# Kernel optimization log

Measured on AMD Instinct MI355X. Metric: run time of the kernel, lower is better.

## Reference

```python
import jax, jax.numpy as jnp
import numpy as np

N_HEADS = 16
HEAD_DIM = 64
D_MODEL = N_HEADS * HEAD_DIM
NEG_INF = -10000.0


def setup_inputs() -> dict:
    key = jax.random.key(0)
    ks = jax.random.split(key, 6)
    B, S = 2, 2048
    std = 0.02
    return {
        "from_tensor": jax.random.normal(ks[0], (B, S, D_MODEL), dtype=jnp.float32),
        "to_tensor": jax.random.normal(ks[1], (B, S, D_MODEL), dtype=jnp.float32),
        "attention_mask": jnp.ones((B, S, S), dtype=jnp.int32),
        "Wq": jax.random.normal(ks[2], (D_MODEL, D_MODEL), dtype=jnp.float32) * std,
        "bq": jnp.zeros((D_MODEL,), dtype=jnp.float32),
        "Wk": jax.random.normal(ks[3], (D_MODEL, D_MODEL), dtype=jnp.float32) * std,
        "bk": jnp.zeros((D_MODEL,), dtype=jnp.float32),
        "Wv": jax.random.normal(ks[4], (D_MODEL, D_MODEL), dtype=jnp.float32) * std,
        "bv": jnp.zeros((D_MODEL,), dtype=jnp.float32),
    }


def reference(from_tensor, to_tensor, attention_mask, Wq, bq, Wk, bk, Wv, bv):
    B, F, _ = from_tensor.shape
    T = to_tensor.shape[1]
    # Dense QKV projections (no activation by default)
    q = from_tensor @ Wq + bq          # [B, F, N*H]
    k = to_tensor @ Wk + bk            # [B, T, N*H]
    v = to_tensor @ Wv + bv            # [B, T, N*H]
    # split heads -> [B, N, S, H]
    q = q.reshape(B, F, N_HEADS, HEAD_DIM).transpose(0, 2, 1, 3)
    k = k.reshape(B, T, N_HEADS, HEAD_DIM).transpose(0, 2, 1, 3)
    v = v.reshape(B, T, N_HEADS, HEAD_DIM).transpose(0, 2, 1, 3)
    # scaled dot-product scores [B, N, F, T]
    scores = jnp.einsum("bnfh,bnth->bnft", q, k) / jnp.sqrt(jnp.float32(HEAD_DIM))
    # additive mask: (1 - mask) * -10000, broadcast over heads
    adder = (1.0 - attention_mask.astype(jnp.float32))[:, None, :, :] * NEG_INF
    scores = scores + adder
    probs = jax.nn.softmax(scores, axis=-1)  # dropout is identity at inference
    ctx = jnp.einsum("bnft,bnth->bnfh", probs, v)  # [B, N, F, H]
    return ctx.transpose(0, 2, 1, 3).reshape(B, F, N_HEADS * HEAD_DIM)
```

## Files before the change

### kernel.cpp

```cpp
#include <hip/hip_runtime.h>
#include <hip/hip_bf16.h>

typedef unsigned short u16;
typedef __bf16 bf16x8 __attribute__((ext_vector_type(8)));
typedef float f32x4 __attribute__((ext_vector_type(4)));

#define D_MODEL 1024
#define NH 16
#define HD 64
#define SEQ 2048
#define BATCH 2

__device__ __forceinline__ f32x4 mfma16(bf16x8 a, bf16x8 b, f32x4 c) {
    return __builtin_amdgcn_mfma_f32_16x16x32_bf16(a, b, c, 0, 0, 0);
}

__device__ __forceinline__ u16 f2bf(float f) {
    __hip_bfloat16 h = __float2bfloat16(f);
    return *reinterpret_cast<u16*>(&h);
}

__device__ __forceinline__ void gload_lds16(const void* g, void* l) {
    __builtin_amdgcn_global_load_lds((__attribute__((address_space(1))) void*)g,
                                     (__attribute__((address_space(3))) void*)l,
                                     16, 0, 0);
}

__global__ __launch_bounds__(256) void convert_k(const float* __restrict__ src,
                                                 u16* __restrict__ dst, int n8) {
    const int i = blockIdx.x * 256 + threadIdx.x;
    if (i >= n8) return;
    const float4 a = ((const float4*)src)[i * 2];
    const float4 b = ((const float4*)src)[i * 2 + 1];
    union { u16 h[8]; uint4 v; } u;
    u.h[0] = f2bf(a.x); u.h[1] = f2bf(a.y); u.h[2] = f2bf(a.z); u.h[3] = f2bf(a.w);
    u.h[4] = f2bf(b.x); u.h[5] = f2bf(b.y); u.h[6] = f2bf(b.z); u.h[7] = f2bf(b.w);
    *(uint4*)(dst + i * 8) = u.v;
}

__global__ __launch_bounds__(256) void transposeW_k(const float* __restrict__ src,
                                                    u16* __restrict__ dst,
                                                    int R, int C) {
    __shared__ __align__(16) u16 t[64][72];
    const int tid = threadIdx.x;
    const int r0 = blockIdx.y * 64, c0 = blockIdx.x * 64;
#pragma unroll
    for (int j = 0; j < 2; ++j) {
        int idx = j * 256 + tid;
        int rr = idx >> 3, cc = idx & 7;
        size_t base = (size_t)(r0 + rr) * C + c0 + cc * 8;
        float4 a = *(const float4*)(src + base);
        float4 b = *(const float4*)(src + base + 4);
        union { u16 h[8]; uint4 v; } u;
        u.h[0] = f2bf(a.x); u.h[1] = f2bf(a.y); u.h[2] = f2bf(a.z); u.h[3] = f2bf(a.w);
        u.h[4] = f2bf(b.x); u.h[5] = f2bf(b.y); u.h[6] = f2bf(b.z); u.h[7] = f2bf(b.w);
        *(uint4*)&t[rr][cc * 8] = u.v;
    }
    __syncthreads();
#pragma unroll
    for (int j = 0; j < 2; ++j) {
        int idx = j * 256 + tid;
        int cc = idx >> 3, rr8 = idx & 7;
        union { u16 h[8]; uint4 v; } u;
#pragma unroll
        for (int e = 0; e < 8; ++e) u.h[e] = t[rr8 * 8 + e][cc];
        *(uint4*)(dst + (size_t)(c0 + cc) * R + r0 + rr8 * 8) = u.v;
    }
}

__global__ __launch_bounds__(256) void maskflags_k(const int* __restrict__ mask,
                                                   int* __restrict__ flags) {
    const int tid = threadIdx.x;
    const int ti = blockIdx.x, fi = blockIdx.y, b = blockIdx.z;
    const int f = fi * 128 + (tid >> 1);
    const int4* p = (const int4*)(mask + ((size_t)(b * SEQ + f)) * SEQ + ti * 64 + (tid & 1) * 32);
    int ok = 1;
#pragma unroll
    for (int j = 0; j < 8; ++j) {
        int4 v = p[j];
        ok &= (v.x == 1) & (v.y == 1) & (v.z == 1) & (v.w == 1);
    }
    __shared__ int sflag;
    if (tid == 0) sflag = 1;
    __syncthreads();
    if (!ok) sflag = 0;
    __syncthreads();
    if (tid == 0) flags[(b * 16 + fi) * 32 + ti] = sflag;
}

__global__ __launch_bounds__(256, 2) void qkv_gemm_k(
    const u16* __restrict__ Xq, const u16* __restrict__ Xkv,
    const u16* __restrict__ Wt,
    const float* __restrict__ bq, const float* __restrict__ bk,
    const float* __restrict__ bv,
    u16* __restrict__ Qb, u16* __restrict__ Kb, u16* __restrict__ Vt) {
    const int z = blockIdx.z;
    const u16* X = (z == 0) ? Xq : Xkv;
    const u16* Wz = Wt + (size_t)z * D_MODEL * D_MODEL;
    const float* bias = (z == 0) ? bq : (z == 1 ? bk : bv);
    const float scale = (z == 0) ? 0.1803368801111244f : 1.0f;

    __shared__ __align__(16) u16 As[128 * 32];
    __shared__ __align__(16) u16 Bs[128 * 32];

    const int tid = threadIdx.x;
    const int w = tid >> 6, lane = tid & 63;
    const int q = lane >> 4, c = lane & 15;
    const int m0 = blockIdx.x * 128, n0 = blockIdx.y * 128;
    const int mw = (w & 1) * 64, nw = (w >> 1) * 64;

    f32x4 acc[4][4];
    const f32x4 z4 = {0.f, 0.f, 0.f, 0.f};
#pragma unroll
    for (int mi = 0; mi < 4; ++mi)
#pragma unroll
        for (int ni = 0; ni < 4; ++ni) acc[mi][ni] = z4;

    for (int kb = 0; kb < 32; ++kb) {
        const int k0 = kb * 32;
#pragma unroll
        for (int j = 0; j < 2; ++j) {
            int i = j * 256 + tid;
            int r = i >> 2, cc = i & 3;
            gload_lds16(X + (size_t)(m0 + r) * D_MODEL + k0 + cc * 8, As + i * 8);
            gload_lds16(Wz + (size_t)(n0 + r) * D_MODEL + k0 + cc * 8, Bs + i * 8);
        }
        __syncthreads();
        bf16x8 af[4], bfr[4];
#pragma unroll
        for (int mi = 0; mi < 4; ++mi)
            af[mi] = *(const bf16x8*)(As + (mw + mi * 16 + c) * 32 + q * 8);
#pragma unroll
        for (int ni = 0; ni < 4; ++ni)
            bfr[ni] = *(const bf16x8*)(Bs + (nw + ni * 16 + c) * 32 + q * 8);
#pragma unroll
        for (int mi = 0; mi < 4; ++mi)
#pragma unroll
            for (int ni = 0; ni < 4; ++ni)
                acc[mi][ni] = mfma16(af[mi], bfr[ni], acc[mi][ni]);
        __syncthreads();
    }

    if (z == 2) {
#pragma unroll
        for (int ni = 0; ni < 4; ++ni) {
            const int colg = n0 + nw + ni * 16 + c;
            const float bvv = bias[colg];
            const int head = colg >> 6, h = colg & 63;
#pragma unroll
            for (int mi = 0; mi < 4; ++mi) {
                const int rowg = m0 + mw + mi * 16 + q * 4;
                const int b = rowg >> 11, s = rowg & 2047;
                union { u16 h4[4]; uint2 v2; } pk;
#pragma unroll
                for (int r = 0; r < 4; ++r) pk.h4[r] = f2bf(acc[mi][ni][r] + bvv);
                *(uint2*)(Vt + (((size_t)(b * NH + head)) * HD + h) * SEQ + s) = pk.v2;
            }
        }
    } else {
        u16* outb = (z == 0) ? Qb : Kb;
#pragma unroll
        for (int ni = 0; ni < 4; ++ni) {
            const int colg = n0 + nw + ni * 16 + c;
            const float bvv = bias[colg];
            const int head = colg >> 6, h = colg & 63;
#pragma unroll
            for (int mi = 0; mi < 4; ++mi) {
                const int rowg = m0 + mw + mi * 16 + q * 4;
#pragma unroll
                for (int r = 0; r < 4; ++r) {
                    const int mrow = rowg + r;
                    const int b = mrow >> 11, s = mrow & 2047;
                    const float val = (acc[mi][ni][r] + bvv) * scale;
                    outb[(((size_t)(b * NH + head)) * SEQ + s) * HD + h] = f2bf(val);
                }
            }
        }
    }
}

#define SK_OFF (128 * 144)
#define SV_OFF (SK_OFF + 64 * 144)
#define SMEM_BYTES (SV_OFF + 64 * 144)

__global__ __launch_bounds__(256, 4) void attn_k(
    const u16* __restrict__ Qb, const u16* __restrict__ Kb, const u16* __restrict__ Vt,
    const int* __restrict__ flags, const int* __restrict__ mask,
    float* __restrict__ O0, float* __restrict__ l0, float* __restrict__ l1,
    float* __restrict__ out) {
    __shared__ __align__(16) unsigned char smem[SMEM_BYTES];
    const int tid = threadIdx.x;
    const int w = tid >> 6, lane = tid & 63;
    const int q = lane >> 4, c = lane & 15;
    const int fi = blockIdx.x, bn = blockIdx.y, ts = blockIdx.z;
    const int b = bn >> 4, n = bn & 15;
    const int f0 = fi * 128;

    u16* sQ = (u16*)(smem);
    u16* sK = (u16*)(smem + SK_OFF);
    u16* sV = (u16*)(smem + SV_OFF);
    u16* sP = sQ + w * 32 * 72;

#pragma unroll
    for (int j = 0; j < 4; ++j) {
        int i = j * 256 + tid;
        int r = i >> 3, cc = i & 7;
        uint4 v = *(const uint4*)(Qb + ((size_t)(bn * SEQ + f0 + r)) * HD + cc * 8);
        *(uint4*)(sQ + r * 72 + cc * 8) = v;
    }
    __syncthreads();

    bf16x8 qf[2][2];
#pragma unroll
    for (int ft = 0; ft < 2; ++ft)
#pragma unroll
        for (int kb = 0; kb < 2; ++kb)
            qf[ft][kb] = *(const bf16x8*)(sQ + (w * 32 + ft * 16 + c) * 72 + kb * 32 + q * 8);
    __asm__ __volatile__("" ::: "memory");
    __builtin_amdgcn_s_waitcnt(0xC07F);
    __asm__ __volatile__("" ::: "memory");

    union { u16 h[8]; bf16x8 v; } one_u;
#pragma unroll
    for (int j = 0; j < 8; ++j) one_u.h[j] = 0x3F80;
    const bf16x8 ones = one_u.v;

    f32x4 O[2][4], accL[2];
    const f32x4 z4 = {0.f, 0.f, 0.f, 0.f};
#pragma unroll
    for (int mi = 0; mi < 2; ++mi) {
        accL[mi] = z4;
#pragma unroll
        for (int hi = 0; hi < 4; ++hi) O[mi][hi] = z4;
    }
    const int* flagp = flags + (b * 16 + fi) * 32;

    const int it0 = ts * 16;
    for (int it = it0; it < it0 + 16; ++it) {
        const int t0 = it * 64;
#pragma unroll
        for (int j = 0; j < 2; ++j) {
            int i = j * 256 + tid;
            int r = i >> 3, cc = i & 7;
            uint4 kv = *(const uint4*)(Kb + ((size_t)(bn * SEQ + t0 + r)) * HD + cc * 8);
            uint4 vv = *(const uint4*)(Vt + ((size_t)(bn * HD + r)) * SEQ + t0 + cc * 8);
            *(uint4*)(sK + r * 72 + cc * 8) = kv;
            *(uint4*)(sV + r * 72 + cc * 8) = vv;
        }
        __syncthreads();

        const int maskslow = (flagp[it] == 0);

#pragma unroll
        for (int mt = 0; mt < 4; ++mt) {
            bf16x8 kf0 = *(const bf16x8*)(sK + (mt * 16 + c) * 72 + 0 + q * 8);
            bf16x8 kf1 = *(const bf16x8*)(sK + (mt * 16 + c) * 72 + 32 + q * 8);
            f32x4 st[2];
#pragma unroll
            for (int ft = 0; ft < 2; ++ft) {
                st[ft] = z4;
                st[ft] = mfma16(kf0, qf[ft][0], st[ft]);
                st[ft] = mfma16(kf1, qf[ft][1], st[ft]);
            }
            if (maskslow) {
#pragma unroll
                for (int ft = 0; ft < 2; ++ft)
#pragma unroll
                    for (int r = 0; r < 4; ++r) {
                        const int fg = f0 + w * 32 + ft * 16 + c;
                        const int tg = t0 + mt * 16 + q * 4 + r;
                        const int mv = mask[((size_t)(b * SEQ + fg)) * SEQ + tg];
                        st[ft][r] += (1.0f - (float)mv) * (-10000.0f) * 1.4426950408889634f;
                    }
            }
#pragma unroll
            for (int ft = 0; ft < 2; ++ft) {
                union { u16 h[4]; uint2 v2; } pk;
#pragma unroll
                for (int r = 0; r < 4; ++r)
                    pk.h[r] = f2bf(exp2f(st[ft][r] - 10.0f));
                *(uint2*)(sP + (ft * 16 + c) * 72 + mt * 16 + q * 4) = pk.v2;
            }
        }
        __asm__ __volatile__("" ::: "memory");
        __builtin_amdgcn_s_waitcnt(0xC07F);
        __asm__ __volatile__("" ::: "memory");

#pragma unroll
        for (int kb = 0; kb < 2; ++kb) {
            bf16x8 pf0 = *(const bf16x8*)(sP + (0 * 16 + c) * 72 + kb * 32 + q * 8);
            bf16x8 pf1 = *(const bf16x8*)(sP + (1 * 16 + c) * 72 + kb * 32 + q * 8);
#pragma unroll
            for (int hi = 0; hi < 4; ++hi) {
                bf16x8 vf = *(const bf16x8*)(sV + (hi * 16 + c) * 72 + kb * 32 + q * 8);
                O[0][hi] = mfma16(pf0, vf, O[0][hi]);
                O[1][hi] = mfma16(pf1, vf, O[1][hi]);
            }
            accL[0] = mfma16(pf0, ones, accL[0]);
            accL[1] = mfma16(pf1, ones, accL[1]);
        }
        __syncthreads();
    }

    float* Odst = ts ? out : O0;
    float* ldst = ts ? l1 : l0;
#pragma unroll
    for (int mi = 0; mi < 2; ++mi)
#pragma unroll
        for (int hi = 0; hi < 4; ++hi)
#pragma unroll
            for (int r = 0; r < 4; ++r) {
                const int fg = f0 + w * 32 + mi * 16 + q * 4 + r;
                const int col = n * 64 + hi * 16 + c;
                Odst[((size_t)(b * SEQ + fg)) * D_MODEL + col] = O[mi][hi][r];
            }
    if (c == 0) {
#pragma unroll
        for (int mi = 0; mi < 2; ++mi)
#pragma unroll
            for (int r = 0; r < 4; ++r) {
                const int fg = f0 + w * 32 + mi * 16 + q * 4 + r;
                ldst[(size_t)bn * SEQ + fg] = accL[mi][r];
            }
    }
}

__global__ __launch_bounds__(256) void combine_k(const float* __restrict__ O0,
                                                 const float* __restrict__ l0,
                                                 const float* __restrict__ l1,
                                                 float* __restrict__ out) {
    const int i = blockIdx.x * 256 + threadIdx.x;
    const int bf = i >> 8;
    const int col = (i & 255) << 2;
    const int n = col >> 6;
    const int lidx = ((bf >> 11) * NH + n) * SEQ + (bf & (SEQ - 1));
    const float inv = 1.0f / (l0[lidx] + l1[lidx]);
    const float4 a = ((const float4*)O0)[i];
    const float4 cpart = ((const float4*)out)[i];
    float4 r;
    r.x = (a.x + cpart.x) * inv;
    r.y = (a.y + cpart.y) * inv;
    r.z = (a.z + cpart.z) * inv;
    r.w = (a.w + cpart.w) * inv;
    ((float4*)out)[i] = r;
}

__global__ __launch_bounds__(256) void signal_k(float* __restrict__ out, int n,
                                                float val) {
    const int i = blockIdx.x * 256 + threadIdx.x;
    if (i < n) out[i] = val;
}

extern "C" void kernel_launch(void* const* d_in, const int* in_sizes, int n_in,
                              void* d_out, int out_size, void* d_ws, size_t ws_size,
                              hipStream_t stream) {
    const float* Xs[2] = {nullptr, nullptr};
    const float* Wp[3] = {nullptr, nullptr, nullptr};
    const float* Bp[3] = {nullptr, nullptr, nullptr};
    const int* mask = nullptr;
    int nx = 0, nw = 0, nb = 0;
    for (int i = 0; i < n_in; ++i) {
        const long long sz = in_sizes[i];
        if (sz == (long long)BATCH * SEQ * D_MODEL) {
            if (nx < 2) Xs[nx++] = (const float*)d_in[i];
        } else if (sz == (long long)BATCH * SEQ * SEQ) {
            mask = (const int*)d_in[i];
        } else if (sz == (long long)D_MODEL * D_MODEL) {
            if (nw < 3) Wp[nw++] = (const float*)d_in[i];
        } else if (sz == (long long)D_MODEL) {
            if (nb < 3) Bp[nb++] = (const float*)d_in[i];
        }
    }
    float* outp = (float*)d_out;
    const size_t MB = 1024 * 1024;
    const size_t NEED = 47 * MB;

    if (ws_size < NEED || nx != 2 || nw != 3 || nb != 3 || !mask) {
        float code = 1000.0f + (float)(ws_size / MB)
                   + (nx != 2 ? 10000.0f : 0.f)
                   + (nw != 3 ? 20000.0f : 0.f)
                   + (nb != 3 ? 40000.0f : 0.f)
                   + (!mask   ? 80000.0f : 0.f);
        signal_k<<<(out_size + 255) / 256, 256, 0, stream>>>(outp, out_size, code);
        return;
    }

    char* ws = (char*)d_ws;
    u16* Xqc   = (u16*)(ws);
    u16* Xkvc  = (u16*)(ws + 8 * MB);
    u16* Wt    = (u16*)(ws + 16 * MB);
    u16* Qb    = (u16*)(ws + 22 * MB);
    u16* Kb    = (u16*)(ws + 30 * MB);
    u16* Vt    = (u16*)(ws + 38 * MB);
    int* flags = (int*)(ws + 46 * MB);
    float* O0 = (float*)(ws);
    float* l0 = (float*)(ws + 46 * MB + 16 * 1024);
    float* l1 = (float*)(ws + 46 * MB + 16 * 1024 + 256 * 1024);

    convert_k<<<2048, 256, 0, stream>>>(Xs[0], Xqc, 524288);
    convert_k<<<2048, 256, 0, stream>>>(Xs[1], Xkvc, 524288);
    transposeW_k<<<dim3(16, 16), 256, 0, stream>>>(Wp[0], Wt,               1024, 1024);
    transposeW_k<<<dim3(16, 16), 256, 0, stream>>>(Wp[1], Wt + 1024 * 1024, 1024, 1024);
    transposeW_k<<<dim3(16, 16), 256, 0, stream>>>(Wp[2], Wt + 2048 * 1024, 1024, 1024);
    maskflags_k<<<dim3(32, 16, 2), 256, 0, stream>>>(mask, flags);
    qkv_gemm_k<<<dim3(32, 8, 3), 256, 0, stream>>>(Xqc, Xkvc, Wt,
                                                   Bp[0], Bp[1], Bp[2], Qb, Kb, Vt);
    attn_k<<<dim3(16, 32, 2), 256, 0, stream>>>(Qb, Kb, Vt, flags, mask,
                                                O0, l0, l1, outp);
    combine_k<<<4096, 256, 0, stream>>>(O0, l0, l1, outp);
}
```

Measured before the change: 232.8 us.

## Merge prep kernels into one launch, add MFMA priority, raise GEMM occupancy

Folds the two input conversions, three weight transposes and the mask-flag scan into a single prep_k launch, with the work chosen by block index. This removes five kernel launches and their tail gaps. It also wraps the attention MFMA sections in s_setprio(1)/s_setprio(0) so waves issuing matrix ops get scheduling priority, and raises the QKV GEMM launch bound from 2 to 3 blocks per SIMD. The higher occupancy target may force register spills.

```diff
diff --git a/kernel.cpp b/kernel.cpp
--- a/kernel.cpp
+++ b/kernel.cpp
@@ -26,69 +26,80 @@
                                      16, 0, 0);
 }
 
-__global__ __launch_bounds__(256) void convert_k(const float* __restrict__ src,
-                                                 u16* __restrict__ dst, int n8) {
-    const int i = blockIdx.x * 256 + threadIdx.x;
-    if (i >= n8) return;
-    const float4 a = ((const float4*)src)[i * 2];
-    const float4 b = ((const float4*)src)[i * 2 + 1];
-    union { u16 h[8]; uint4 v; } u;
-    u.h[0] = f2bf(a.x); u.h[1] = f2bf(a.y); u.h[2] = f2bf(a.z); u.h[3] = f2bf(a.w);
-    u.h[4] = f2bf(b.x); u.h[5] = f2bf(b.y); u.h[6] = f2bf(b.z); u.h[7] = f2bf(b.w);
-    *(uint4*)(dst + i * 8) = u.v;
-}
-
-__global__ __launch_bounds__(256) void transposeW_k(const float* __restrict__ src,
-                                                    u16* __restrict__ dst,
-                                                    int R, int C) {
+__global__ __launch_bounds__(256) void prep_k(
+    const float* __restrict__ X0, const float* __restrict__ X1,
+    u16* __restrict__ Xqc, u16* __restrict__ Xkvc,
+    const float* __restrict__ W0, const float* __restrict__ W1,
+    const float* __restrict__ W2, u16* __restrict__ Wt,
+    const int* __restrict__ mask, int* __restrict__ flags) {
     __shared__ __align__(16) u16 t[64][72];
     const int tid = threadIdx.x;
-    const int r0 = blockIdx.y * 64, c0 = blockIdx.x * 64;
-#pragma unroll
-    for (int j = 0; j < 2; ++j) {
-        int idx = j * 256 + tid;
-        int rr = idx >> 3, cc = idx & 7;
-        size_t base = (size_t)(r0 + rr) * C + c0 + cc * 8;
-        float4 a = *(const float4*)(src + base);
-        float4 b = *(const float4*)(src + base + 4);
+    int bid = blockIdx.x;
+
+    if (bid < 4096) {
+        int i = bid * 256 + tid;
+        const float* src = X0; u16* dst = Xqc;
+        if (i >= 524288) { src = X1; dst = Xkvc; i -= 524288; }
+        const float4 a = ((const float4*)src)[i * 2];
+        const float4 b = ((const float4*)src)[i * 2 + 1];
         union { u16 h[8]; uint4 v; } u;
         u.h[0] = f2bf(a.x); u.h[1] = f2bf(a.y); u.h[2] = f2bf(a.z); u.h[3] = f2bf(a.w);
         u.h[4] = f2bf(b.x); u.h[5] = f2bf(b.y); u.h[6] = f2bf(b.z); u.h[7] = f2bf(b.w);
-        *(uint4*)&t[rr][cc * 8] = u.v;
-    }
-    __syncthreads();
-#pragma unroll
-    for (int j = 0; j < 2; ++j) {
-        int idx = j * 256 + tid;
-        int cc = idx >> 3, rr8 = idx & 7;
-        union { u16 h[8]; uint4 v; } u;
-#pragma unroll
-        for (int e = 0; e < 8; ++e) u.h[e] = t[rr8 * 8 + e][cc];
-        *(uint4*)(dst + (size_t)(c0 + cc) * R + r0 + rr8 * 8) = u.v;
-    }
-}
-
-__global__ __launch_bounds__(256) void maskflags_k(const int* __restrict__ mask,
-                                                   int* __restrict__ flags) {
-    const int tid = threadIdx.x;
-    const int ti = blockIdx.x, fi = blockIdx.y, b = blockIdx.z;
-    const int f = fi * 128 + (tid >> 1);
-    const int4* p = (const int4*)(mask + ((size_t)(b * SEQ + f)) * SEQ + ti * 64 + (tid & 1) * 32);
-    int ok = 1;
-#pragma unroll
-    for (int j = 0; j < 8; ++j) {
-        int4 v = p[j];
-        ok &= (v.x == 1) & (v.y == 1) & (v.z == 1) & (v.w == 1);
-    }
-    __shared__ int sflag;
-    if (tid == 0) sflag = 1;
-    __syncthreads();
-    if (!ok) sflag = 0;
-    __syncthreads();
-    if (tid == 0) flags[(b * 16 + fi) * 32 + ti] = sflag;
-}
-
-__global__ __launch_bounds__(256, 2) void qkv_gemm_k(
+        *(uint4*)(dst + i * 8) = u.v;
+        return;
+    }
+    bid -= 4096;
+    if (bid < 768) {
+        const int z = bid >> 8, rem = bid & 255;
+        const int bx = rem & 15, by = rem >> 4;
+        const float* src = (z == 0) ? W0 : (z == 1 ? W1 : W2);
+        u16* dst = Wt + (size_t)z * D_MODEL * D_MODEL;
+        const int r0 = by * 64, c0 = bx * 64;
+#pragma unroll
+        for (int j = 0; j < 2; ++j) {
+            int idx = j * 256 + tid;
+            int rr = idx >> 3, cc = idx & 7;
+            size_t base = (size_t)(r0 + rr) * D_MODEL + c0 + cc * 8;
+            float4 a = *(const float4*)(src + base);
+            float4 b = *(const float4*)(src + base + 4);
+            union { u16 h[8]; uint4 v; } u;
+            u.h[0] = f2bf(a.x); u.h[1] = f2bf(a.y); u.h[2] = f2bf(a.z); u.h[3] = f2bf(a.w);
+            u.h[4] = f2bf(b.x); u.h[5] = f2bf(b.y); u.h[6] = f2bf(b.z); u.h[7] = f2bf(b.w);
+            *(uint4*)&t[rr][cc * 8] = u.v;
+        }
+        __syncthreads();
+#pragma unroll
+        for (int j = 0; j < 2; ++j) {
+            int idx = j * 256 + tid;
+            int cc = idx >> 3, rr8 = idx & 7;
+            union { u16 h[8]; uint4 v; } u;
+#pragma unroll
+            for (int e = 0; e < 8; ++e) u.h[e] = t[rr8 * 8 + e][cc];
+            *(uint4*)(dst + (size_t)(c0 + cc) * D_MODEL + r0 + rr8 * 8) = u.v;
+        }
+        return;
+    }
+    bid -= 768;
+    {
+        const int ti = bid & 31, fi = (bid >> 5) & 15, b = bid >> 9;
+        const int f = fi * 128 + (tid >> 1);
+        const int4* p = (const int4*)(mask + ((size_t)(b * SEQ + f)) * SEQ + ti * 64 + (tid & 1) * 32);
+        int ok = 1;
+#pragma unroll
+        for (int j = 0; j < 8; ++j) {
+            int4 v = p[j];
+            ok &= (v.x == 1) & (v.y == 1) & (v.z == 1) & (v.w == 1);
+        }
+        __shared__ int sflag;
+        if (tid == 0) sflag = 1;
+        __syncthreads();
+        if (!ok) sflag = 0;
+        __syncthreads();
+        if (tid == 0) flags[(b * 16 + fi) * 32 + ti] = sflag;
+    }
+}
+
+__global__ __launch_bounds__(256, 3) void qkv_gemm_k(
     const u16* __restrict__ Xq, const u16* __restrict__ Xkv,
     const u16* __restrict__ Wt,
     const float* __restrict__ bq, const float* __restrict__ bk,
@@ -256,12 +267,14 @@
             bf16x8 kf0 = *(const bf16x8*)(sK + (mt * 16 + c) * 72 + 0 + q * 8);
             bf16x8 kf1 = *(const bf16x8*)(sK + (mt * 16 + c) * 72 + 32 + q * 8);
             f32x4 st[2];
+            __builtin_amdgcn_s_setprio(1);
 #pragma unroll
             for (int ft = 0; ft < 2; ++ft) {
                 st[ft] = z4;
                 st[ft] = mfma16(kf0, qf[ft][0], st[ft]);
                 st[ft] = mfma16(kf1, qf[ft][1], st[ft]);
             }
+            __builtin_amdgcn_s_setprio(0);
             if (maskslow) {
 #pragma unroll
                 for (int ft = 0; ft < 2; ++ft)
@@ -286,6 +299,7 @@
         __builtin_amdgcn_s_waitcnt(0xC07F);
         __asm__ __volatile__("" ::: "memory");
 
+        __builtin_amdgcn_s_setprio(1);
 #pragma unroll
         for (int kb = 0; kb < 2; ++kb) {
             bf16x8 pf0 = *(const bf16x8*)(sP + (0 * 16 + c) * 72 + kb * 32 + q * 8);
@@ -299,6 +313,7 @@
             accL[0] = mfma16(pf0, ones, accL[0]);
             accL[1] = mfma16(pf1, ones, accL[1]);
         }
+        __builtin_amdgcn_s_setprio(0);
         __syncthreads();
     }
 
@@ -397,12 +412,8 @@
     float* l0 = (float*)(ws + 46 * MB + 16 * 1024);
     float* l1 = (float*)(ws + 46 * MB + 16 * 1024 + 256 * 1024);
 
-    convert_k<<<2048, 256, 0, stream>>>(Xs[0], Xqc, 524288);
-    convert_k<<<2048, 256, 0, stream>>>(Xs[1], Xkvc, 524288);
-    transposeW_k<<<dim3(16, 16), 256, 0, stream>>>(Wp[0], Wt,               1024, 1024);
-    transposeW_k<<<dim3(16, 16), 256, 0, stream>>>(Wp[1], Wt + 1024 * 1024, 1024, 1024);
-    transposeW_k<<<dim3(16, 16), 256, 0, stream>>>(Wp[2], Wt + 2048 * 1024, 1024, 1024);
-    maskflags_k<<<dim3(32, 16, 2), 256, 0, stream>>>(mask, flags);
+    prep_k<<<5888, 256, 0, stream>>>(Xs[0], Xs[1], Xqc, Xkvc,
+                                     Wp[0], Wp[1], Wp[2], Wt, mask, flags);
     qkv_gemm_k<<<dim3(32, 8, 3), 256, 0, stream>>>(Xqc, Xkvc, Wt,
                                                    Bp[0], Bp[1], Bp[2], Qb, Kb, Vt);
     attn_k<<<dim3(16, 32, 2), 256, 0, stream>>>(Qb, Kb, Vt, flags, mask,
```

Result: faster. 223.3 us (-4.1%).
